# Optimization experiments

Measured on AMD Instinct MI355X. Metric: run time of the kernel, lower is better.

Reference implementation:

```python
import jax, jax.numpy as jnp
import numpy as np

B = 16384
IN_FEATURES = 256
OUT_FEATURES = 4096
CH_GROUP = 8
NUM_SLICE = IN_FEATURES // CH_GROUP  # 32


def setup_inputs() -> dict:
    key = jax.random.key(0)
    kx, kw = jax.random.split(key)
    x = jax.random.normal(kx, (B, IN_FEATURES), dtype=jnp.float32)
    # Stacked weights of the 32 tiny Linear(ch_group -> out_features, bias=False)
    # layers; W[i] corresponds to fc_i.weight with shape [out_features, ch_group].
    W = jax.random.normal(kw, (NUM_SLICE, OUT_FEATURES, CH_GROUP), dtype=jnp.float32) * (1.0 / np.sqrt(CH_GROUP))
    return {"x": x, "W": W}


def reference(x, W):
    # Equivalent to sum_i fc_i(x[:, i*cg:(i+1)*cg]) = fused block GEMM.
    xs = x.reshape(x.shape[0], NUM_SLICE, CH_GROUP)  # [B, S, C]
    # out[b,o] = sum_{s,c} xs[b,s,c] * W[s,o,c]
    return jnp.einsum('bsc,soc->bo', xs, W)
```

## Files before the change

kernel.cpp:

```cpp
#include <hip/hip_runtime.h>
#include <hip/hip_bf16.h>


typedef __attribute__((ext_vector_type(8)))  __bf16          bf16x8;
typedef __attribute__((ext_vector_type(8)))  unsigned short  ushort8;
typedef __attribute__((ext_vector_type(4)))  float           floatx4;

__device__ __forceinline__ unsigned short f2bf(float f) {
    union { float f; unsigned u; } v; v.f = f;
    unsigned r = v.u + 0x7fffu + ((v.u >> 16) & 1u);
    return (unsigned short)(r >> 16);
}

__global__ void conv_x_kernel(const float* __restrict__ x,
                              unsigned short* __restrict__ xb) {
    const int t = blockIdx.x * 256 + threadIdx.x;
    const float4* p = (const float4*)x;
    float4 a = p[2 * t], b = p[2 * t + 1];
    ushort8 v;
    v[0] = f2bf(a.x); v[1] = f2bf(a.y); v[2] = f2bf(a.z); v[3] = f2bf(a.w);
    v[4] = f2bf(b.x); v[5] = f2bf(b.y); v[6] = f2bf(b.z); v[7] = f2bf(b.w);
    *(ushort8*)(xb + (size_t)t * 8) = v;
}

__global__ void pack_w_kernel(const float* __restrict__ W,
                              unsigned short* __restrict__ wb) {
    const int t = blockIdx.x * 256 + threadIdx.x;
    const int s = t >> 12;
    const int o = t & 4095;
    const float4* p = (const float4*)(W + (size_t)s * 32768 + (size_t)o * 8);
    float4 a = p[0], b = p[1];
    ushort8 v;
    v[0] = f2bf(a.x); v[1] = f2bf(a.y); v[2] = f2bf(a.z); v[3] = f2bf(a.w);
    v[4] = f2bf(b.x); v[5] = f2bf(b.y); v[6] = f2bf(b.z); v[7] = f2bf(b.w);
    *(ushort8*)(wb + (size_t)o * 256 + (size_t)s * 8) = v;
}

__device__ __forceinline__ void gload_lds16(const unsigned short* g, unsigned short* l) {
    __builtin_amdgcn_global_load_lds(
        (const __attribute__((address_space(1))) unsigned int*)(const void*)g,
        (__attribute__((address_space(3))) unsigned int*)(void*)l,
        16, 0, 0);
}

__global__ __launch_bounds__(256) void gemm_kernel(
    const unsigned short* __restrict__ A,
    const unsigned short* __restrict__ Bt,
    float* __restrict__ C) {
    __shared__ __align__(16) unsigned short lsA[128 * 32];
    __shared__ __align__(16) unsigned short lsB[128 * 32];

    const int tid  = threadIdx.x;
    const int wave = tid >> 6;
    const int lane = tid & 63;
    const int bm   = blockIdx.y;
    const int bn   = blockIdx.x;

    const int sr  = tid >> 2;
    const int scc = ((tid & 3) ^ ((tid >> 3) & 3)) * 8;
    const unsigned short* Ag = A  + ((size_t)(bm * 128 + sr)) * 256 + scc;
    const unsigned short* Bg = Bt + ((size_t)(bn * 128 + sr)) * 256 + scc;

    unsigned short* lA0 = &lsA[wave * 512];
    unsigned short* lA1 = &lsA[2048 + wave * 512];
    unsigned short* lB0 = &lsB[wave * 512];
    unsigned short* lB1 = &lsB[2048 + wave * 512];

    const int wrow = wave >> 1, wcol = wave & 1;
    const int fr = lane & 15;
    const int fq = lane >> 4;
    const int cs = (fq ^ ((fr >> 1) & 3)) * 8;
    const unsigned short* aF = &lsA[(wrow * 64 + fr) * 32] + cs;
    const unsigned short* bF = &lsB[(wcol * 64 + fr) * 32] + cs;

    floatx4 acc[4][4] = {};

    for (int kt = 0; kt < 8; ++kt) {
        const int ko = kt * 32;
        gload_lds16(Ag + ko,             lA0);
        gload_lds16(Ag + ko + 64 * 256,  lA1);
        gload_lds16(Bg + ko,             lB0);
        gload_lds16(Bg + ko + 64 * 256,  lB1);
        __syncthreads();

        bf16x8 af[4], bfv[4];
#pragma unroll
        for (int i = 0; i < 4; ++i) {
            af[i]  = *(const bf16x8*)(const void*)(aF + i * 16 * 32);
            bfv[i] = *(const bf16x8*)(const void*)(bF + i * 16 * 32);
        }
#pragma unroll
        for (int i = 0; i < 4; ++i)
#pragma unroll
            for (int j = 0; j < 4; ++j)
                acc[i][j] = __builtin_amdgcn_mfma_f32_16x16x32_bf16(
                    af[i], bfv[j], acc[i][j], 0, 0, 0);
        __syncthreads();
    }

    const int row0 = bm * 128 + wrow * 64 + fq * 4;
    const int col0 = bn * 128 + wcol * 64 + fr;
#pragma unroll
    for (int i = 0; i < 4; ++i) {
#pragma unroll
        for (int j = 0; j < 4; ++j) {
            float* Cp = C + (size_t)(row0 + i * 16) * 4096 + col0 + j * 16;
#pragma unroll
            for (int r = 0; r < 4; ++r)
                Cp[(size_t)r * 4096] = acc[i][j][r];
        }
    }
}

extern "C" void kernel_launch(void* const* d_in, const int* in_sizes, int n_in,
                              void* d_out, int out_size, void* d_ws, size_t ws_size,
                              hipStream_t stream) {
    const float* x = (const float*)d_in[0];
    const float* W = (const float*)d_in[1];
    float* out = (float*)d_out;

    unsigned short* xb = (unsigned short*)d_ws;
    unsigned short* wb = xb + (size_t)16384 * 256;

    conv_x_kernel<<<2048, 256, 0, stream>>>(x, xb);
    pack_w_kernel<<<512, 256, 0, stream>>>(W, wb);

    dim3 grid(32, 128);
    gemm_kernel<<<grid, 256, 0, stream>>>(xb, wb, out);
}
```

Measured before the change: 298.4 us.

## Double-buffer LDS tiles in GEMM and use nontemporal output stores

```diff
diff --git a/kernel.cpp b/kernel.cpp
--- a/kernel.cpp
+++ b/kernel.cpp
@@ -47,8 +47,8 @@
     const unsigned short* __restrict__ A,
     const unsigned short* __restrict__ Bt,
     float* __restrict__ C) {
-    __shared__ __align__(16) unsigned short lsA[128 * 32];
-    __shared__ __align__(16) unsigned short lsB[128 * 32];
+    __shared__ __align__(16) unsigned short lsA[2][128 * 32];
+    __shared__ __align__(16) unsigned short lsB[2][128 * 32];
 
     const int tid  = threadIdx.x;
     const int wave = tid >> 6;
@@ -61,28 +61,37 @@
     const unsigned short* Ag = A  + ((size_t)(bm * 128 + sr)) * 256 + scc;
     const unsigned short* Bg = Bt + ((size_t)(bn * 128 + sr)) * 256 + scc;
 
-    unsigned short* lA0 = &lsA[wave * 512];
-    unsigned short* lA1 = &lsA[2048 + wave * 512];
-    unsigned short* lB0 = &lsB[wave * 512];
-    unsigned short* lB1 = &lsB[2048 + wave * 512];
+    const int so0 = wave * 512;
+    const int so1 = 2048 + wave * 512;
 
     const int wrow = wave >> 1, wcol = wave & 1;
     const int fr = lane & 15;
     const int fq = lane >> 4;
     const int cs = (fq ^ ((fr >> 1) & 3)) * 8;
-    const unsigned short* aF = &lsA[(wrow * 64 + fr) * 32] + cs;
-    const unsigned short* bF = &lsB[(wcol * 64 + fr) * 32] + cs;
+    const int offA = (wrow * 64 + fr) * 32 + cs;
+    const int offB = (wcol * 64 + fr) * 32 + cs;
 
     floatx4 acc[4][4] = {};
 
+    gload_lds16(Ag,            &lsA[0][so0]);
+    gload_lds16(Ag + 64 * 256, &lsA[0][so1]);
+    gload_lds16(Bg,            &lsB[0][so0]);
+    gload_lds16(Bg + 64 * 256, &lsB[0][so1]);
+
     for (int kt = 0; kt < 8; ++kt) {
-        const int ko = kt * 32;
-        gload_lds16(Ag + ko,             lA0);
-        gload_lds16(Ag + ko + 64 * 256,  lA1);
-        gload_lds16(Bg + ko,             lB0);
-        gload_lds16(Bg + ko + 64 * 256,  lB1);
+        const int cur = kt & 1;
         __syncthreads();
+        if (kt < 7) {
+            const int nxt = cur ^ 1;
+            const int ko  = (kt + 1) * 32;
+            gload_lds16(Ag + ko,            &lsA[nxt][so0]);
+            gload_lds16(Ag + ko + 64 * 256, &lsA[nxt][so1]);
+            gload_lds16(Bg + ko,            &lsB[nxt][so0]);
+            gload_lds16(Bg + ko + 64 * 256, &lsB[nxt][so1]);
+        }
 
+        const unsigned short* aF = &lsA[cur][offA];
+        const unsigned short* bF = &lsB[cur][offB];
         bf16x8 af[4], bfv[4];
 #pragma unroll
         for (int i = 0; i < 4; ++i) {
@@ -95,7 +104,6 @@
             for (int j = 0; j < 4; ++j)
                 acc[i][j] = __builtin_amdgcn_mfma_f32_16x16x32_bf16(
                     af[i], bfv[j], acc[i][j], 0, 0, 0);
-        __syncthreads();
     }
 
     const int row0 = bm * 128 + wrow * 64 + fq * 4;
@@ -107,7 +115,7 @@
             float* Cp = C + (size_t)(row0 + i * 16) * 4096 + col0 + j * 16;
 #pragma unroll
             for (int r = 0; r < 4; ++r)
-                Cp[(size_t)r * 4096] = acc[i][j][r];
+                __builtin_nontemporal_store(acc[i][j][r], Cp + (size_t)r * 4096);
         }
     }
 }
```

Measured after the change: 301.5 us. Within noise of the previous version (+1.0%).

## Pre-pack operands into MFMA fragment layout and load directly to registers

Applied to the files above, without the earlier changes.

```diff
diff --git a/kernel.cpp b/kernel.cpp
--- a/kernel.cpp
+++ b/kernel.cpp
@@ -12,92 +12,82 @@
     return (unsigned short)(r >> 16);
 }
 
-__global__ void conv_x_kernel(const float* __restrict__ x,
-                              unsigned short* __restrict__ xb) {
-    const int t = blockIdx.x * 256 + threadIdx.x;
-    const float4* p = (const float4*)x;
-    float4 a = p[2 * t], b = p[2 * t + 1];
-    ushort8 v;
-    v[0] = f2bf(a.x); v[1] = f2bf(a.y); v[2] = f2bf(a.z); v[3] = f2bf(a.w);
-    v[4] = f2bf(b.x); v[5] = f2bf(b.y); v[6] = f2bf(b.z); v[7] = f2bf(b.w);
-    *(ushort8*)(xb + (size_t)t * 8) = v;
-}
-
-__global__ void pack_w_kernel(const float* __restrict__ W,
-                              unsigned short* __restrict__ wb) {
-    const int t = blockIdx.x * 256 + threadIdx.x;
-    const int s = t >> 12;
-    const int o = t & 4095;
-    const float4* p = (const float4*)(W + (size_t)s * 32768 + (size_t)o * 8);
+__global__ void pack_x_kernel(const float* __restrict__ x,
+                              unsigned short* __restrict__ A2) {
+    const int u    = blockIdx.x * 256 + threadIdx.x;
+    const int lane = u & 63;
+    const int kc   = (u >> 6) & 7;
+    const int mt   = u >> 9;
+    const int r    = mt * 16 + (lane & 15);
+    const int k    = kc * 32 + (lane >> 4) * 8;
+    const float4* p = (const float4*)(x + (size_t)r * 256 + k);
     float4 a = p[0], b = p[1];
     ushort8 v;
     v[0] = f2bf(a.x); v[1] = f2bf(a.y); v[2] = f2bf(a.z); v[3] = f2bf(a.w);
     v[4] = f2bf(b.x); v[5] = f2bf(b.y); v[6] = f2bf(b.z); v[7] = f2bf(b.w);
-    *(ushort8*)(wb + (size_t)o * 256 + (size_t)s * 8) = v;
+    *(ushort8*)(A2 + (size_t)u * 8) = v;
 }
 
-__device__ __forceinline__ void gload_lds16(const unsigned short* g, unsigned short* l) {
-    __builtin_amdgcn_global_load_lds(
-        (const __attribute__((address_space(1))) unsigned int*)(const void*)g,
-        (__attribute__((address_space(3))) unsigned int*)(void*)l,
-        16, 0, 0);
+__global__ void pack_w_kernel(const float* __restrict__ W,
+                              unsigned short* __restrict__ B2) {
+    const int u    = blockIdx.x * 256 + threadIdx.x;
+    const int lane = u & 63;
+    const int kc   = (u >> 6) & 7;
+    const int nt   = u >> 9;
+    const int o    = nt * 16 + (lane & 15);
+    const int s    = kc * 4 + (lane >> 4);
+    const float4* p = (const float4*)(W + ((size_t)s * 4096 + o) * 8);
+    float4 a = p[0], b = p[1];
+    ushort8 v;
+    v[0] = f2bf(a.x); v[1] = f2bf(a.y); v[2] = f2bf(a.z); v[3] = f2bf(a.w);
+    v[4] = f2bf(b.x); v[5] = f2bf(b.y); v[6] = f2bf(b.z); v[7] = f2bf(b.w);
+    *(ushort8*)(B2 + (size_t)u * 8) = v;
 }
 
 __global__ __launch_bounds__(256) void gemm_kernel(
-    const unsigned short* __restrict__ A,
-    const unsigned short* __restrict__ Bt,
+    const unsigned short* __restrict__ A2,
+    const unsigned short* __restrict__ B2,
     float* __restrict__ C) {
-    __shared__ __align__(16) unsigned short lsA[128 * 32];
-    __shared__ __align__(16) unsigned short lsB[128 * 32];
-
     const int tid  = threadIdx.x;
     const int wave = tid >> 6;
     const int lane = tid & 63;
     const int bm   = blockIdx.y;
     const int bn   = blockIdx.x;
+    const int wrow = wave >> 1, wcol = wave & 1;
 
-    const int sr  = tid >> 2;
-    const int scc = ((tid & 3) ^ ((tid >> 3) & 3)) * 8;
-    const unsigned short* Ag = A  + ((size_t)(bm * 128 + sr)) * 256 + scc;
-    const unsigned short* Bg = Bt + ((size_t)(bn * 128 + sr)) * 256 + scc;
-
-    unsigned short* lA0 = &lsA[wave * 512];
-    unsigned short* lA1 = &lsA[2048 + wave * 512];
-    unsigned short* lB0 = &lsB[wave * 512];
-    unsigned short* lB1 = &lsB[2048 + wave * 512];
-
-    const int wrow = wave >> 1, wcol = wave & 1;
-    const int fr = lane & 15;
-    const int fq = lane >> 4;
-    const int cs = (fq ^ ((fr >> 1) & 3)) * 8;
-    const unsigned short* aF = &lsA[(wrow * 64 + fr) * 32] + cs;
-    const unsigned short* bF = &lsB[(wcol * 64 + fr) * 32] + cs;
+    const unsigned short* Ab = A2 + ((size_t)(bm * 8 + wrow * 4) * 4096) + lane * 8;
+    const unsigned short* Bb = B2 + ((size_t)(bn * 8 + wcol * 4) * 4096) + lane * 8;
 
     floatx4 acc[4][4] = {};
+    bf16x8 af[2][4], bf[2][4];
 
-    for (int kt = 0; kt < 8; ++kt) {
-        const int ko = kt * 32;
-        gload_lds16(Ag + ko,             lA0);
-        gload_lds16(Ag + ko + 64 * 256,  lA1);
-        gload_lds16(Bg + ko,             lB0);
-        gload_lds16(Bg + ko + 64 * 256,  lB1);
-        __syncthreads();
+#pragma unroll
+    for (int i = 0; i < 4; ++i) {
+        af[0][i] = *(const bf16x8*)(const void*)(Ab + i * 4096);
+        bf[0][i] = *(const bf16x8*)(const void*)(Bb + i * 4096);
+    }
 
-        bf16x8 af[4], bfv[4];
 #pragma unroll
-        for (int i = 0; i < 4; ++i) {
-            af[i]  = *(const bf16x8*)(const void*)(aF + i * 16 * 32);
-            bfv[i] = *(const bf16x8*)(const void*)(bF + i * 16 * 32);
+    for (int kc = 0; kc < 8; ++kc) {
+        const int cur = kc & 1, nxt = cur ^ 1;
+        if (kc < 7) {
+            const int ko = (kc + 1) * 512;
+#pragma unroll
+            for (int i = 0; i < 4; ++i) {
+                af[nxt][i] = *(const bf16x8*)(const void*)(Ab + i * 4096 + ko);
+                bf[nxt][i] = *(const bf16x8*)(const void*)(Bb + i * 4096 + ko);
+            }
         }
 #pragma unroll
         for (int i = 0; i < 4; ++i)
 #pragma unroll
             for (int j = 0; j < 4; ++j)
                 acc[i][j] = __builtin_amdgcn_mfma_f32_16x16x32_bf16(
-                    af[i], bfv[j], acc[i][j], 0, 0, 0);
-        __syncthreads();
+                    af[cur][i], bf[cur][j], acc[i][j], 0, 0, 0);
     }
 
+    const int fr = lane & 15;
+    const int fq = lane >> 4;
     const int row0 = bm * 128 + wrow * 64 + fq * 4;
     const int col0 = bn * 128 + wcol * 64 + fr;
 #pragma unroll
@@ -107,7 +97,7 @@
             float* Cp = C + (size_t)(row0 + i * 16) * 4096 + col0 + j * 16;
 #pragma unroll
             for (int r = 0; r < 4; ++r)
-                Cp[(size_t)r * 4096] = acc[i][j][r];
+                __builtin_nontemporal_store(acc[i][j][r], Cp + (size_t)r * 4096);
         }
     }
 }
@@ -119,12 +109,12 @@
     const float* W = (const float*)d_in[1];
     float* out = (float*)d_out;
 
-    unsigned short* xb = (unsigned short*)d_ws;
-    unsigned short* wb = xb + (size_t)16384 * 256;
+    unsigned short* A2 = (unsigned short*)d_ws;
+    unsigned short* B2 = A2 + (size_t)16384 * 256;
 
-    conv_x_kernel<<<2048, 256, 0, stream>>>(x, xb);
-    pack_w_kernel<<<512, 256, 0, stream>>>(W, wb);
+    pack_x_kernel<<<2048, 256, 0, stream>>>(x, A2);
+    pack_w_kernel<<<512, 256, 0, stream>>>(W, B2);
 
     dim3 grid(32, 128);
-    gemm_kernel<<<grid, 256, 0, stream>>>(xb, wb, out);
+    gemm_kernel<<<grid, 256, 0, stream>>>(A2, B2, out);
 }
```

Result: slower. 307.1 us (+2.9%).
